# Performance work log

Hardware: AMD Instinct MI355X
Metric: run time of the kernel (lower is better)

Reference implementation:

```python
import jax, jax.numpy as jnp
import numpy as np

DIM, HID, SEQ = 768, 2048, 4096
LR, MOM, WD, THRESH = 1e-3, 0.9, 0.01, 0.1


def _net(p, x):
    W1, b1, W2, b2, W3, b3, W4, b4 = p
    h = jax.nn.relu(x @ W1 + b1)
    h = jax.nn.relu(h @ W2 + b2)
    h = jax.nn.relu(h @ W3 + b3)
    return h @ W4 + b4


def _loss(p, t):
    # t: [dim]; token.unsqueeze(0) then mse_loss (mean over all elements)
    pred = _net(p, t[None, :])
    return jnp.mean((pred - t[None, :]) ** 2)


def _ttt(params, x):
    toks = x[::4]  # `if i % 4 != 0: continue`

    def step(carry, t):
        p, buf, inited = carry
        g = jax.grad(_loss)(p, t)
        surprise = sum(jnp.linalg.norm(gi) for gi in jax.tree_util.tree_leaves(g))
        # momentum buffer: first observation initializes it
        buf_new = jnp.where(inited, MOM * buf + (1.0 - MOM) * surprise, surprise)

        def upd(q):
            qd = jax.tree_util.tree_map(lambda w: w * (1.0 - WD), q)  # weight decay
            g2 = jax.grad(_loss)(qd, t)                                # fresh fwd/bwd
            return jax.tree_util.tree_map(lambda w, gi: w - LR * gi, qd, g2)  # SGD step

        p_new = jax.lax.cond(buf_new > THRESH, upd, lambda q: q, p)
        return (p_new, buf_new, jnp.bool_(True)), None

    (pf, _, _), _ = jax.lax.scan(step, (params, jnp.float32(0.0), jnp.bool_(False)), toks)
    return pf


def setup_inputs() -> dict:
    key = jax.random.key(0)
    ks = jax.random.split(key, 5)

    def lin(k, fi, fo):
        kw, kb = jax.random.split(k)
        w = jax.random.normal(kw, (fi, fo), jnp.float32) / np.sqrt(fi).astype(np.float32)
        b = jax.random.normal(kb, (fo,), jnp.float32) * 0.01
        return w, b

    W1, b1 = lin(ks[0], DIM, HID)
    W2, b2 = lin(ks[1], HID, HID)
    W3, b3 = lin(ks[2], HID, HID)
    W4, b4 = lin(ks[3], HID, DIM)
    x = jax.random.normal(ks[4], (SEQ, DIM), jnp.float32)
    return dict(x=x, W1=W1, b1=b1, W2=W2, b2=b2, W3=W3, b3=b3, W4=W4, b4=b4, do_ttt=1)


def reference(x, W1, b1, W2, b2, W3, b3, W4, b4, do_ttt):
    params = (W1, b1, W2, b2, W3, b3, W4, b4)
    if do_ttt:
        params = _ttt(params, x)
    out = _net(params, x)            # eval pass over full sequence
    return out.mean(axis=0, keepdims=True)  # memory_summary [1, dim]
```

## Files before the change

### kernel.cpp

```cpp
#include <hip/hip_runtime.h>
#include <cstddef>

#define LRC 0.001f
#define DEC 0.99f

static const size_t OFF_Z1P = 0;
static const size_t OFF_Z2P = 65536;
static const size_t OFF_Z2Q = 131072;
static const size_t OFF_Z3P = 196608;
static const size_t OFF_Z3Q = 262144;
static const size_t OFF_Z4P = 327680;
static const size_t OFF_Z4Q = 352256;
static const size_t OFF_H1F = 376832;
static const size_t OFF_H1Q = 378880;
static const size_t OFF_H2F = 380928;
static const size_t OFF_H2Q = 382976;
static const size_t OFF_H3F = 385024;
static const size_t OFF_H3Q = 387072;
static const size_t OFF_D4F = 389120;
static const size_t OFF_D4Q = 389888;
static const size_t OFF_D3F = 390656;
static const size_t OFF_D3Q = 392704;
static const size_t OFF_D2F = 394752;
static const size_t OFF_D2Q = 396800;
static const size_t OFF_D1F = 398848;
static const size_t OFF_D1Q = 400896;
static const size_t OFF_NSQ = 402944;
static const size_t OFF_SL3 = 402960;
static const size_t OFF_SL2 = 403216;
static const size_t OFF_SL1 = 403472;
static const size_t OFF_BUF = 403728;
static const size_t OFF_CONDF = 403730;
static const size_t OFF_MSUM = 403732;
static const size_t OFF_HA  = 428308;
static const size_t OFF_HB  = 2525460;

__device__ inline void fma4(float4& a, float s, const float4& w) {
    a.x += s * w.x; a.y += s * w.y; a.z += s * w.z; a.w += s * w.w;
}

__device__ float block_reduce_512(float v) {
    __shared__ float red[512];
    int t = threadIdx.x;
    red[t] = v;
    __syncthreads();
    for (int s = 256; s > 0; s >>= 1) {
        if (t < s) red[t] += red[t + s];
        __syncthreads();
    }
    float r = red[0];
    __syncthreads();
    return r;
}

__global__ __launch_bounds__(512) void k_fwd1(int step,
                                              const float* __restrict__ xt,
                                              const float* __restrict__ xprev,
                                              float* __restrict__ W1,
                                              float* __restrict__ b1,
                                              float* __restrict__ wsf,
                                              const int* __restrict__ flag) {
    if (*flag == 0) return;
    int b = blockIdx.x;
    int g = b >> 5, p = b & 31;
    int tid = threadIdx.x, w = tid >> 6, lane = tid & 63;
    int c0 = g * 256 + lane * 4;
    int kb = p * 24 + w * 3;

    float4 wv0 = *(const float4*)(W1 + (size_t)(kb + 0) * 2048 + c0);
    float4 wv1 = *(const float4*)(W1 + (size_t)(kb + 1) * 2048 + c0);
    float4 wv2 = *(const float4*)(W1 + (size_t)(kb + 2) * 2048 + c0);
    float a0 = xt[kb + 0], a1 = xt[kb + 1], a2 = xt[kb + 2];
    float4 dv = make_float4(0.f, 0.f, 0.f, 0.f);
    float u0 = 0.f, u1 = 0.f, u2 = 0.f;
    if (step > 0) {
        dv = *(const float4*)(wsf + OFF_D1Q + c0);
        u0 = LRC * xprev[kb + 0]; u1 = LRC * xprev[kb + 1]; u2 = LRC * xprev[kb + 2];
    }

    __shared__ float cnd[4];
    float cond = 0.f;
    if (step > 0) {
        if (w < 3) {
            const float* sl = wsf + (w == 0 ? OFF_SL1 : (w == 1 ? OFF_SL2 : OFF_SL3));
            float v = sl[lane] + sl[lane + 64] + sl[lane + 128] + sl[lane + 192];
#pragma unroll
            for (int off = 32; off > 0; off >>= 1) v += __shfl_down(v, off);
            if (lane == 0) cnd[w] = v;
        }
        __syncthreads();
        float nd1 = sqrtf(cnd[0]), nd2 = sqrtf(cnd[1]), nd3 = sqrtf(cnd[2]);
        float nx = sqrtf(wsf[OFF_NSQ + 0]);
        float nh1 = sqrtf(wsf[OFF_NSQ + 1]);
        float nh2 = sqrtf(wsf[OFF_NSQ + 2]);
        float nh3 = sqrtf(wsf[OFF_NSQ + 3]);
        float nd4 = sqrtf(wsf[OFF_NSQ + 4]);
        float surprise = nx * nd1 + nd1 + nh1 * nd2 + nd2 + nh2 * nd3 + nd3 + nh3 * nd4 + nd4;
        float bufold = wsf[OFF_BUF + ((step - 1) & 1)];
        float bufnew = (step == 1) ? surprise : (0.9f * bufold + 0.1f * surprise);
        cond = (bufnew > 0.1f) ? 1.f : 0.f;
        if (b == 0 && tid == 0) {
            wsf[OFF_BUF + (step & 1)] = bufnew;
            wsf[OFF_CONDF] = cond;
        }
    } else {
        if (b == 0 && tid == 0) wsf[OFF_CONDF] = 0.f;
    }

    if (cond != 0.f) {
        wv0.x = DEC * wv0.x - u0 * dv.x; wv0.y = DEC * wv0.y - u0 * dv.y;
        wv0.z = DEC * wv0.z - u0 * dv.z; wv0.w = DEC * wv0.w - u0 * dv.w;
        wv1.x = DEC * wv1.x - u1 * dv.x; wv1.y = DEC * wv1.y - u1 * dv.y;
        wv1.z = DEC * wv1.z - u1 * dv.z; wv1.w = DEC * wv1.w - u1 * dv.w;
        wv2.x = DEC * wv2.x - u2 * dv.x; wv2.y = DEC * wv2.y - u2 * dv.y;
        wv2.z = DEC * wv2.z - u2 * dv.z; wv2.w = DEC * wv2.w - u2 * dv.w;
        *(float4*)(W1 + (size_t)(kb + 0) * 2048 + c0) = wv0;
        *(float4*)(W1 + (size_t)(kb + 1) * 2048 + c0) = wv1;
        *(float4*)(W1 + (size_t)(kb + 2) * 2048 + c0) = wv2;
        if (b == 0) {
            int c = tid * 4;
            float4 dq = *(const float4*)(wsf + OFF_D1Q + c);
            float4 bv = *(float4*)(b1 + c);
            bv.x = DEC * bv.x - LRC * dq.x; bv.y = DEC * bv.y - LRC * dq.y;
            bv.z = DEC * bv.z - LRC * dq.z; bv.w = DEC * bv.w - LRC * dq.w;
            *(float4*)(b1 + c) = bv;
        }
    }

    float4 acc = make_float4(0.f, 0.f, 0.f, 0.f);
    fma4(acc, a0, wv0); fma4(acc, a1, wv1); fma4(acc, a2, wv2);

    __shared__ float4 red[8][64];
    red[w][lane] = acc;
    __syncthreads();
    if (w == 0) {
        float4 s = red[0][lane];
#pragma unroll
        for (int q = 1; q < 8; ++q) {
            float4 r2 = red[q][lane];
            s.x += r2.x; s.y += r2.y; s.z += r2.z; s.w += r2.w;
        }
        *(float4*)(wsf + OFF_Z1P + (size_t)p * 2048 + c0) = s;
    }
}

__global__ __launch_bounds__(512) void k_fwd2(const float* __restrict__ zinP,
                                              const float* __restrict__ zinQ,
                                              const float* __restrict__ bin,
                                              float* __restrict__ W, int Nout,
                                              float* __restrict__ zoutP,
                                              float* __restrict__ zoutQ,
                                              const float* __restrict__ uprev,
                                              const float* __restrict__ vprev,
                                              float* __restrict__ bl,
                                              const float* __restrict__ wsf,
                                              const int* __restrict__ flag) {
    if (*flag == 0) return;
    int b = blockIdx.x;
    int g = b >> 5, p = b & 31;
    int tid = threadIdx.x, w = tid >> 6, lane = tid & 63;
    bool upd = (wsf[OFF_CONDF] != 0.f);

    __shared__ float hs[64], hq[64], us[64];
    if (tid < 64) {
        int k = p * 64 + tid;
        float s = 0.f;
#pragma unroll 8
        for (int pp = 0; pp < 32; ++pp) s += zinP[pp * 2048 + k];
        float bv = bin[k];
        float h = fmaxf(s + bv, 0.f);
        float hqq;
        if (zinQ) {
            float sq = 0.f;
#pragma unroll 8
            for (int pp = 0; pp < 32; ++pp) sq += zinQ[pp * 2048 + k];
            hqq = fmaxf(DEC * (sq + bv), 0.f);
        } else {
            hqq = DEC * h;
        }
        hs[tid] = h; hq[tid] = hqq;
        us[tid] = upd ? (LRC * uprev[k]) : 0.f;
    }
    __syncthreads();
    int c0 = g * 256 + lane * 4;
    float4 vpv = make_float4(0.f, 0.f, 0.f, 0.f);
    if (upd) vpv = *(const float4*)(vprev + c0);
    float4 ap = make_float4(0.f, 0.f, 0.f, 0.f);
    float4 aq = make_float4(0.f, 0.f, 0.f, 0.f);
    if (upd) {
#pragma unroll
        for (int r = 0; r < 8; ++r) {
            int kk = w * 8 + r;
            float* wp = W + (size_t)(p * 64 + kk) * Nout + c0;
            float4 wv = *(const float4*)wp;
            float u = us[kk];
            wv.x = DEC * wv.x - u * vpv.x; wv.y = DEC * wv.y - u * vpv.y;
            wv.z = DEC * wv.z - u * vpv.z; wv.w = DEC * wv.w - u * vpv.w;
            *(float4*)wp = wv;
            float a = hs[kk], a2 = hq[kk];
            fma4(ap, a, wv);
            fma4(aq, a2, wv);
        }
    } else {
#pragma unroll
        for (int r = 0; r < 8; ++r) {
            int kk = w * 8 + r;
            const float4 wv = *(const float4*)(W + (size_t)(p * 64 + kk) * Nout + c0);
            float a = hs[kk], a2 = hq[kk];
            fma4(ap, a, wv);
            fma4(aq, a2, wv);
        }
    }
    if (upd && b == 0) {
        int c = tid * 4;
        if (c < Nout) {
            float4 dq = *(const float4*)(vprev + c);
            float4 bv = *(float4*)(bl + c);
            bv.x = DEC * bv.x - LRC * dq.x; bv.y = DEC * bv.y - LRC * dq.y;
            bv.z = DEC * bv.z - LRC * dq.z; bv.w = DEC * bv.w - LRC * dq.w;
            *(float4*)(bl + c) = bv;
        }
    }
    __shared__ float4 redP[8][64];
    __shared__ float4 redQ[8][64];
    redP[w][lane] = ap; redQ[w][lane] = aq;
    __syncthreads();
    if (w == 0) {
        float4 sp = redP[0][lane], sq4 = redQ[0][lane];
#pragma unroll
        for (int q = 1; q < 8; ++q) {
            float4 r2 = redP[q][lane]; sp.x += r2.x; sp.y += r2.y; sp.z += r2.z; sp.w += r2.w;
            float4 r3 = redQ[q][lane]; sq4.x += r3.x; sq4.y += r3.y; sq4.z += r3.z; sq4.w += r3.w;
        }
        *(float4*)(zoutP + (size_t)p * Nout + c0) = sp;
        *(float4*)(zoutQ + (size_t)p * Nout + c0) = sq4;
    }
}

__global__ __launch_bounds__(512) void k_fin(float* __restrict__ wsf,
                                             const float* __restrict__ xt,
                                             const float* __restrict__ b1,
                                             const float* __restrict__ b2,
                                             const float* __restrict__ b3,
                                             const float* __restrict__ b4,
                                             const int* __restrict__ flag) {
    if (*flag == 0) return;
    int b = blockIdx.x, tid = threadIdx.x;
    if (b < 16) {
        if (tid < 128) {
            int e = b * 128 + tid;
            float s = 0.f;
#pragma unroll 8
            for (int pp = 0; pp < 32; ++pp) s += wsf[OFF_Z1P + pp * 2048 + e];
            float h = fmaxf(s + b1[e], 0.f);
            wsf[OFF_H1F + e] = h;
            wsf[OFF_H1Q + e] = DEC * h;
        }
    } else if (b < 32) {
        if (tid < 128) {
            int e = (b - 16) * 128 + tid;
            float s = 0.f, sq = 0.f;
#pragma unroll 8
            for (int pp = 0; pp < 32; ++pp) {
                s += wsf[OFF_Z2P + pp * 2048 + e];
                sq += wsf[OFF_Z2Q + pp * 2048 + e];
            }
            float bv = b2[e];
            wsf[OFF_H2F + e] = fmaxf(s + bv, 0.f);
            wsf[OFF_H2Q + e] = fmaxf(DEC * (sq + bv), 0.f);
        }
    } else if (b < 48) {
        if (tid < 128) {
            int e = (b - 32) * 128 + tid;
            float s = 0.f, sq = 0.f;
#pragma unroll 8
            for (int pp = 0; pp < 32; ++pp) {
                s += wsf[OFF_Z3P + pp * 2048 + e];
                sq += wsf[OFF_Z3Q + pp * 2048 + e];
            }
            float bv = b3[e];
            wsf[OFF_H3F + e] = fmaxf(s + bv, 0.f);
            wsf[OFF_H3Q + e] = fmaxf(DEC * (sq + bv), 0.f);
        }
    } else if (b == 48) {
        for (int e = tid; e < 768; e += 512) {
            float s = 0.f, sq = 0.f;
#pragma unroll 8
            for (int pp = 0; pp < 32; ++pp) {
                s += wsf[OFF_Z4P + pp * 768 + e];
                sq += wsf[OFF_Z4Q + pp * 768 + e];
            }
            float bv = b4[e], tv = xt[e];
            float pred = s + bv;
            float predq = DEC * (sq + bv);
            wsf[OFF_D4F + e] = 2.f * (pred - tv) * (1.f / 768.f);
            wsf[OFF_D4Q + e] = 2.f * (predq - tv) * (1.f / 768.f);
        }
    } else if (b == 49) {
        float v = 0.f;
        for (int e = tid; e < 768; e += 512) { float xv = xt[e]; v += xv * xv; }
        float s = block_reduce_512(v);
        if (tid == 0) wsf[OFF_NSQ + 0] = s;
    } else if (b == 50) {
        float v = 0.f;
        for (int e = tid; e < 2048; e += 512) {
            float s = 0.f;
#pragma unroll 8
            for (int pp = 0; pp < 32; ++pp) s += wsf[OFF_Z1P + pp * 2048 + e];
            float h = fmaxf(s + b1[e], 0.f);
            v += h * h;
        }
        float s = block_reduce_512(v);
        if (tid == 0) wsf[OFF_NSQ + 1] = s;
    } else if (b == 51) {
        float v = 0.f;
        for (int e = tid; e < 2048; e += 512) {
            float s = 0.f;
#pragma unroll 8
            for (int pp = 0; pp < 32; ++pp) s += wsf[OFF_Z2P + pp * 2048 + e];
            float h = fmaxf(s + b2[e], 0.f);
            v += h * h;
        }
        float s = block_reduce_512(v);
        if (tid == 0) wsf[OFF_NSQ + 2] = s;
    } else if (b == 52) {
        float v = 0.f;
        for (int e = tid; e < 2048; e += 512) {
            float s = 0.f;
#pragma unroll 8
            for (int pp = 0; pp < 32; ++pp) s += wsf[OFF_Z3P + pp * 2048 + e];
            float h = fmaxf(s + b3[e], 0.f);
            v += h * h;
        }
        float s = block_reduce_512(v);
        if (tid == 0) wsf[OFF_NSQ + 3] = s;
    } else if (b == 53) {
        float v = 0.f;
        for (int e = tid; e < 768; e += 512) {
            float s = 0.f;
#pragma unroll 8
            for (int pp = 0; pp < 32; ++pp) s += wsf[OFF_Z4P + pp * 768 + e];
            float d = 2.f * ((s + b4[e]) - xt[e]) * (1.f / 768.f);
            v += d * d;
        }
        float s = block_reduce_512(v);
        if (tid == 0) wsf[OFF_NSQ + 4] = s;
    }
}

__global__ __launch_bounds__(512) void k_bwd(const float* __restrict__ W, int K,
                                             const float* __restrict__ dinP,
                                             const float* __restrict__ dinQ,
                                             const float* __restrict__ hP,
                                             const float* __restrict__ hQ,
                                             float* __restrict__ doutP,
                                             float* __restrict__ doutQ,
                                             float* __restrict__ slot,
                                             const int* __restrict__ flag) {
    if (*flag == 0) return;
    __shared__ float dsP[2048];
    __shared__ float dsQ[2048];
    int tid = threadIdx.x;
    for (int k = tid; k < K; k += 512) { dsP[k] = dinP[k]; dsQ[k] = dinQ[k]; }
    __syncthreads();
    int w = tid >> 6, lane = tid & 63;
    int j = blockIdx.x * 8 + w;
    const float* row = W + (size_t)j * K;
    float ap = 0.f, aq = 0.f;
    for (int k4 = lane * 4; k4 < K; k4 += 256) {
        const float4 wv = *(const float4*)(row + k4);
        ap += wv.x * dsP[k4] + wv.y * dsP[k4 + 1] + wv.z * dsP[k4 + 2] + wv.w * dsP[k4 + 3];
        aq += wv.x * dsQ[k4] + wv.y * dsQ[k4 + 1] + wv.z * dsQ[k4 + 2] + wv.w * dsQ[k4 + 3];
    }
#pragma unroll
    for (int off = 32; off > 0; off >>= 1) {
        ap += __shfl_down(ap, off);
        aq += __shfl_down(aq, off);
    }
    __shared__ float sqw[8];
    if (lane == 0) {
        float dp = (hP[j] > 0.f) ? ap : 0.f;
        float dq = (hQ[j] > 0.f) ? DEC * aq : 0.f;
        doutP[j] = dp;
        doutQ[j] = dq;
        sqw[w] = dp * dp;
    }
    __syncthreads();
    if (tid == 0) {
        float s = 0.f;
#pragma unroll
        for (int q = 0; q < 8; ++q) s += sqw[q];
        slot[blockIdx.x] = s;
    }
}

__global__ __launch_bounds__(512) void k_upd(int step, float* __restrict__ wsf,
                                             float* __restrict__ W1, float* __restrict__ b1,
                                             float* __restrict__ W2, float* __restrict__ b2,
                                             float* __restrict__ W3, float* __restrict__ b3,
                                             float* __restrict__ W4, float* __restrict__ b4,
                                             const float* __restrict__ xt,
                                             const int* __restrict__ flag) {
    if (*flag == 0) return;
    int tid = threadIdx.x, b = blockIdx.x;
    float s3 = block_reduce_512((tid < 256) ? wsf[OFF_SL3 + tid] : 0.f);
    float s2 = block_reduce_512((tid < 256) ? wsf[OFF_SL2 + tid] : 0.f);
    float s1 = block_reduce_512((tid < 256) ? wsf[OFF_SL1 + tid] : 0.f);
    __shared__ float condsh;
    if (tid == 0) {
        float nx = sqrtf(wsf[OFF_NSQ + 0]);
        float nh1 = sqrtf(wsf[OFF_NSQ + 1]);
        float nh2 = sqrtf(wsf[OFF_NSQ + 2]);
        float nh3 = sqrtf(wsf[OFF_NSQ + 3]);
        float nd4 = sqrtf(wsf[OFF_NSQ + 4]);
        float nd3 = sqrtf(s3), nd2 = sqrtf(s2), nd1 = sqrtf(s1);
        float surprise = nx * nd1 + nd1 + nh1 * nd2 + nd2 + nh2 * nd3 + nd3 + nh3 * nd4 + nd4;
        float bufold = wsf[OFF_BUF + (step & 1)];
        float bufnew = (step == 0) ? surprise : (0.9f * bufold + 0.1f * surprise);
        wsf[OFF_BUF + ((step + 1) & 1)] = bufnew;
        condsh = (bufnew > 0.1f) ? 1.f : 0.f;
    }
    __syncthreads();
    if (condsh == 0.f) return;

    const float* d1q = wsf + OFF_D1Q;
    const float* d2q = wsf + OFF_D2Q;
    const float* d3q = wsf + OFF_D3Q;
    const float* d4q = wsf + OFF_D4Q;
    const float* h1q = wsf + OFF_H1Q;
    const float* h2q = wsf + OFF_H2Q;
    const float* h3q = wsf + OFF_H3Q;
    int c = tid * 4;
    {
        float4 dv = *(const float4*)(d1q + c);
#pragma unroll
        for (int r = 0; r < 3; ++r) {
            int i = b * 3 + r;
            float u = LRC * xt[i];
            float4* wp = (float4*)(W1 + (size_t)i * 2048 + c);
            float4 wv = *wp;
            wv.x = DEC * wv.x - u * dv.x; wv.y = DEC * wv.y - u * dv.y;
            wv.z = DEC * wv.z - u * dv.z; wv.w = DEC * wv.w - u * dv.w;
            *wp = wv;
        }
    }
    {
        float4 dv = *(const float4*)(d2q + c);
#pragma unroll
        for (int r = 0; r < 8; ++r) {
            int i = b * 8 + r;
            float u = LRC * h1q[i];
            float4* wp = (float4*)(W2 + (size_t)i * 2048 + c);
            float4 wv = *wp;
            wv.x = DEC * wv.x - u * dv.x; wv.y = DEC * wv.y - u * dv.y;
            wv.z = DEC * wv.z - u * dv.z; wv.w = DEC * wv.w - u * dv.w;
            *wp = wv;
        }
    }
    {
        float4 dv = *(const float4*)(d3q + c);
#pragma unroll
        for (int r = 0; r < 8; ++r) {
            int i = b * 8 + r;
            float u = LRC * h2q[i];
            float4* wp = (float4*)(W3 + (size_t)i * 2048 + c);
            float4 wv = *wp;
            wv.x = DEC * wv.x - u * dv.x; wv.y = DEC * wv.y - u * dv.y;
            wv.z = DEC * wv.z - u * dv.z; wv.w = DEC * wv.w - u * dv.w;
            *wp = wv;
        }
    }
    if (tid < 192) {
        float4 dv = *(const float4*)(d4q + c);
#pragma unroll
        for (int r = 0; r < 8; ++r) {
            int i = b * 8 + r;
            float u = LRC * h3q[i];
            float4* wp = (float4*)(W4 + (size_t)i * 768 + c);
            float4 wv = *wp;
            wv.x = DEC * wv.x - u * dv.x; wv.y = DEC * wv.y - u * dv.y;
            wv.z = DEC * wv.z - u * dv.z; wv.w = DEC * wv.w - u * dv.w;
            *wp = wv;
        }
    }
    if (b == 0) {
        float4 dv = *(const float4*)(d1q + c);
        float4* bp = (float4*)(b1 + c);
        float4 bv = *bp;
        bv.x = DEC * bv.x - LRC * dv.x; bv.y = DEC * bv.y - LRC * dv.y;
        bv.z = DEC * bv.z - LRC * dv.z; bv.w = DEC * bv.w - LRC * dv.w;
        *bp = bv;
    } else if (b == 1) {
        float4 dv = *(const float4*)(d2q + c);
        float4* bp = (float4*)(b2 + c);
        float4 bv = *bp;
        bv.x = DEC * bv.x - LRC * dv.x; bv.y = DEC * bv.y - LRC * dv.y;
        bv.z = DEC * bv.z - LRC * dv.z; bv.w = DEC * bv.w - LRC * dv.w;
        *bp = bv;
    } else if (b == 2) {
        float4 dv = *(const float4*)(d3q + c);
        float4* bp = (float4*)(b3 + c);
        float4 bv = *bp;
        bv.x = DEC * bv.x - LRC * dv.x; bv.y = DEC * bv.y - LRC * dv.y;
        bv.z = DEC * bv.z - LRC * dv.z; bv.w = DEC * bv.w - LRC * dv.w;
        *bp = bv;
    } else if (b == 3 && tid < 192) {
        float4 dv = *(const float4*)(d4q + c);
        float4* bp = (float4*)(b4 + c);
        float4 bv = *bp;
        bv.x = DEC * bv.x - LRC * dv.x; bv.y = DEC * bv.y - LRC * dv.y;
        bv.z = DEC * bv.z - LRC * dv.z; bv.w = DEC * bv.w - LRC * dv.w;
        *bp = bv;
    }
}

__global__ __launch_bounds__(256) void k_gemm(const float* __restrict__ A,
                                              const float* __restrict__ W,
                                              const float* __restrict__ bias,
                                              float* __restrict__ C,
                                              int M, int N, int K, int do_relu) {
    __shared__ float sA[16][64];
    __shared__ float sB[16][128];
    int bn = blockIdx.x, bm = blockIdx.y;
    int m0 = bm * 64, n0 = bn * 128;
    int tid = threadIdx.x;
    int tx = tid & 31, ty = tid >> 5;
    float acc[8][4];
#pragma unroll
    for (int i = 0; i < 8; ++i)
#pragma unroll
        for (int j = 0; j < 4; ++j) acc[i][j] = 0.f;

    for (int kt = 0; kt < K; kt += 16) {
        {
            int r = tid >> 2, cc = (tid & 3) * 4;
            const float4 a4 = *(const float4*)(A + (size_t)(m0 + r) * K + kt + cc);
            sA[cc + 0][r] = a4.x; sA[cc + 1][r] = a4.y; sA[cc + 2][r] = a4.z; sA[cc + 3][r] = a4.w;
        }
        {
            int r = tid >> 5, cc = (tid & 31) * 4;
            *(float4*)(&sB[r][cc]) = *(const float4*)(W + (size_t)(kt + r) * N + n0 + cc);
            *(float4*)(&sB[r + 8][cc]) = *(const float4*)(W + (size_t)(kt + r + 8) * N + n0 + cc);
        }
        __syncthreads();
#pragma unroll
        for (int k = 0; k < 16; ++k) {
            float av[8];
#pragma unroll
            for (int i = 0; i < 8; ++i) av[i] = sA[k][ty * 8 + i];
            float bx = sB[k][tx * 4 + 0], by = sB[k][tx * 4 + 1];
            float bz = sB[k][tx * 4 + 2], bw = sB[k][tx * 4 + 3];
#pragma unroll
            for (int i = 0; i < 8; ++i) {
                acc[i][0] += av[i] * bx; acc[i][1] += av[i] * by;
                acc[i][2] += av[i] * bz; acc[i][3] += av[i] * bw;
            }
        }
        __syncthreads();
    }
    float bx = bias[n0 + tx * 4 + 0], by = bias[n0 + tx * 4 + 1];
    float bz = bias[n0 + tx * 4 + 2], bw = bias[n0 + tx * 4 + 3];
#pragma unroll
    for (int i = 0; i < 8; ++i) {
        int m = m0 + ty * 8 + i;
        float4 v;
        v.x = acc[i][0] + bx; v.y = acc[i][1] + by;
        v.z = acc[i][2] + bz; v.w = acc[i][3] + bw;
        if (do_relu) {
            v.x = fmaxf(v.x, 0.f); v.y = fmaxf(v.y, 0.f);
            v.z = fmaxf(v.z, 0.f); v.w = fmaxf(v.w, 0.f);
        }
        *(float4*)(C + (size_t)m * N + n0 + tx * 4) = v;
    }
}

__global__ __launch_bounds__(128) void k_colsum(const float* __restrict__ Y,
                                                float* __restrict__ out) {
    int c = blockIdx.x * 128 + threadIdx.x;
    int r0 = blockIdx.y * 128;
    float s = 0.f;
    for (int r = 0; r < 128; ++r) s += Y[(size_t)(r0 + r) * 768 + c];
    out[blockIdx.y * 768 + c] = s;
}

__global__ __launch_bounds__(768) void k_out(const float* __restrict__ msum,
                                             float* __restrict__ out) {
    int c = threadIdx.x;
    float s = 0.f;
#pragma unroll
    for (int i = 0; i < 32; ++i) s += msum[i * 768 + c];
    out[c] = s * (1.f / 4096.f);
}

extern "C" void kernel_launch(void* const* d_in, const int* in_sizes, int n_in,
                              void* d_out, int out_size, void* d_ws, size_t ws_size,
                              hipStream_t stream) {
    const float* x = (const float*)d_in[0];
    float* W1 = (float*)d_in[1];
    float* b1 = (float*)d_in[2];
    float* W2 = (float*)d_in[3];
    float* b2 = (float*)d_in[4];
    float* W3 = (float*)d_in[5];
    float* b3 = (float*)d_in[6];
    float* W4 = (float*)d_in[7];
    float* b4 = (float*)d_in[8];
    const int* flag = (const int*)d_in[9];
    float* wsf = (float*)d_ws;

    for (int s = 0; s < 1024; ++s) {
        const float* xt = x + (size_t)s * 4 * 768;
        const float* xprev = x + (size_t)(s > 0 ? s - 1 : 0) * 4 * 768;
        k_fwd1<<<256, 512, 0, stream>>>(s, xt, xprev, W1, b1, wsf, flag);
        k_fwd2<<<256, 512, 0, stream>>>(wsf + OFF_Z1P, nullptr, b1, W2, 2048,
                                        wsf + OFF_Z2P, wsf + OFF_Z2Q,
                                        wsf + OFF_H1Q, wsf + OFF_D2Q, b2, wsf, flag);
        k_fwd2<<<256, 512, 0, stream>>>(wsf + OFF_Z2P, wsf + OFF_Z2Q, b2, W3, 2048,
                                        wsf + OFF_Z3P, wsf + OFF_Z3Q,
                                        wsf + OFF_H2Q, wsf + OFF_D3Q, b3, wsf, flag);
        k_fwd2<<<96, 512, 0, stream>>>(wsf + OFF_Z3P, wsf + OFF_Z3Q, b3, W4, 768,
                                       wsf + OFF_Z4P, wsf + OFF_Z4Q,
                                       wsf + OFF_H3Q, wsf + OFF_D4Q, b4, wsf, flag);
        k_fin<<<64, 512, 0, stream>>>(wsf, xt, b1, b2, b3, b4, flag);
        k_bwd<<<256, 512, 0, stream>>>(W4, 768, wsf + OFF_D4F, wsf + OFF_D4Q,
                                       wsf + OFF_H3F, wsf + OFF_H3Q,
                                       wsf + OFF_D3F, wsf + OFF_D3Q, wsf + OFF_SL3, flag);
        k_bwd<<<256, 512, 0, stream>>>(W3, 2048, wsf + OFF_D3F, wsf + OFF_D3Q,
                                       wsf + OFF_H2F, wsf + OFF_H2Q,
                                       wsf + OFF_D2F, wsf + OFF_D2Q, wsf + OFF_SL2, flag);
        k_bwd<<<256, 512, 0, stream>>>(W2, 2048, wsf + OFF_D2F, wsf + OFF_D2Q,
                                       wsf + OFF_H1F, wsf + OFF_H1Q,
                                       wsf + OFF_D1F, wsf + OFF_D1Q, wsf + OFF_SL1, flag);
    }
    k_upd<<<256, 512, 0, stream>>>(1023, wsf, W1, b1, W2, b2, W3, b3, W4, b4,
                                   x + (size_t)1023 * 4 * 768, flag);

    float* HA = wsf + OFF_HA;
    float* HB = wsf + OFF_HB;
    for (int ch = 0; ch < 4; ++ch) {
        const float* Xc = x + (size_t)ch * 1024 * 768;
        k_gemm<<<dim3(16, 16), 256, 0, stream>>>(Xc, W1, b1, HA, 1024, 2048, 768, 1);
        k_gemm<<<dim3(16, 16), 256, 0, stream>>>(HA, W2, b2, HB, 1024, 2048, 2048, 1);
        k_gemm<<<dim3(16, 16), 256, 0, stream>>>(HB, W3, b3, HA, 1024, 2048, 2048, 1);
        k_gemm<<<dim3(6, 16), 256, 0, stream>>>(HA, W4, b4, HB, 1024, 768, 2048, 0);
        k_colsum<<<dim3(6, 8), 128, 0, stream>>>(HB, wsf + OFF_MSUM + (size_t)ch * 8 * 768);
    }
    k_out<<<1, 768, 0, stream>>>(wsf + OFF_MSUM, (float*)d_out);
}
```

Baseline: 64.93 ms.

## Fuse per-step TTT kernels into one persistent kernel with grid barriers

Replaces the roughly 8 kernel launches per scan step (over 8000 in total) with a single persistent 256-block kernel that moves between phases through a hierarchical atomic grid barrier. The finalize phase is spread across idle blocks during the layer-4 forward, and the layer-4 backward is fused with the computation of its output gradient. The goal is to remove per-launch overhead and the gaps between launches. In exchange it depends on all 256 blocks being resident at once, and each step now pays the cost of spinning on global atomic barriers.

Measured after the change: 211.7 ms. 226% more time.

```diff
diff --git a/kernel.cpp b/kernel.cpp
--- a/kernel.cpp
+++ b/kernel.cpp
@@ -3,6 +3,7 @@
 
 #define LRC 0.001f
 #define DEC 0.99f
+#define NBLK 256
 
 static const size_t OFF_Z1P = 0;
 static const size_t OFF_Z2P = 65536;
@@ -35,17 +36,16 @@
 static const size_t OFF_HA  = 428308;
 static const size_t OFF_HB  = 2525460;
 
-__device__ inline void fma4(float4& a, float s, const float4& w) {
+__device__ __forceinline__ void fma4(float4& a, float s, const float4& w) {
     a.x += s * w.x; a.y += s * w.y; a.z += s * w.z; a.w += s * w.w;
 }
 
-__device__ float block_reduce_512(float v) {
-    __shared__ float red[512];
+__device__ __forceinline__ float block_reduce_512s(float v, float* red) {
     int t = threadIdx.x;
     red[t] = v;
     __syncthreads();
-    for (int s = 256; s > 0; s >>= 1) {
-        if (t < s) red[t] += red[t + s];
+    for (int st = 256; st > 0; st >>= 1) {
+        if (t < st) red[t] += red[t + st];
         __syncthreads();
     }
     float r = red[0];
@@ -53,14 +53,35 @@
     return r;
 }
 
-__global__ __launch_bounds__(512) void k_fwd1(int step,
-                                              const float* __restrict__ xt,
-                                              const float* __restrict__ xprev,
-                                              float* __restrict__ W1,
-                                              float* __restrict__ b1,
-                                              float* __restrict__ wsf,
-                                              const int* __restrict__ flag) {
-    if (*flag == 0) return;
+__device__ __forceinline__ void gbar(unsigned* bar) {
+    __syncthreads();
+    if (threadIdx.x == 0) {
+        __threadfence();
+        unsigned g = __hip_atomic_load(bar, __ATOMIC_RELAXED, __HIP_MEMORY_SCOPE_AGENT);
+        unsigned* grp = bar + 64 + ((blockIdx.x >> 4) << 5);
+        if (__hip_atomic_fetch_add(grp, 1u, __ATOMIC_ACQ_REL, __HIP_MEMORY_SCOPE_AGENT) == 15u) {
+            if (__hip_atomic_fetch_add(bar + 32, 1u, __ATOMIC_ACQ_REL, __HIP_MEMORY_SCOPE_AGENT) == 15u) {
+#pragma unroll
+                for (int i = 0; i < 16; ++i)
+                    __hip_atomic_store(bar + 64 + (i << 5), 0u, __ATOMIC_RELAXED, __HIP_MEMORY_SCOPE_AGENT);
+                __hip_atomic_store(bar + 32, 0u, __ATOMIC_RELAXED, __HIP_MEMORY_SCOPE_AGENT);
+                __hip_atomic_store(bar, g + 1u, __ATOMIC_RELEASE, __HIP_MEMORY_SCOPE_AGENT);
+            }
+        }
+        while (__hip_atomic_load(bar, __ATOMIC_RELAXED, __HIP_MEMORY_SCOPE_AGENT) == g)
+            __builtin_amdgcn_s_sleep(2);
+        __threadfence();
+    }
+    __syncthreads();
+}
+
+__device__ __forceinline__ void ph_fwd1(int step,
+                                        const float* __restrict__ xt,
+                                        const float* __restrict__ xprev,
+                                        float* __restrict__ W1,
+                                        float* __restrict__ b1,
+                                        float* __restrict__ wsf,
+                                        float* smem) {
     int b = blockIdx.x;
     int g = b >> 5, p = b & 31;
     int tid = threadIdx.x, w = tid >> 6, lane = tid & 63;
@@ -78,7 +99,7 @@
         u0 = LRC * xprev[kb + 0]; u1 = LRC * xprev[kb + 1]; u2 = LRC * xprev[kb + 2];
     }
 
-    __shared__ float cnd[4];
+    float* cnd = smem + 2048;
     float cond = 0.f;
     if (step > 0) {
         if (w < 3) {
@@ -130,38 +151,37 @@
     float4 acc = make_float4(0.f, 0.f, 0.f, 0.f);
     fma4(acc, a0, wv0); fma4(acc, a1, wv1); fma4(acc, a2, wv2);
 
-    __shared__ float4 red[8][64];
-    red[w][lane] = acc;
+    float4* red4 = (float4*)smem;
+    red4[w * 64 + lane] = acc;
     __syncthreads();
     if (w == 0) {
-        float4 s = red[0][lane];
+        float4 s = red4[lane];
 #pragma unroll
         for (int q = 1; q < 8; ++q) {
-            float4 r2 = red[q][lane];
+            float4 r2 = red4[q * 64 + lane];
             s.x += r2.x; s.y += r2.y; s.z += r2.z; s.w += r2.w;
         }
         *(float4*)(wsf + OFF_Z1P + (size_t)p * 2048 + c0) = s;
     }
 }
 
-__global__ __launch_bounds__(512) void k_fwd2(const float* __restrict__ zinP,
-                                              const float* __restrict__ zinQ,
-                                              const float* __restrict__ bin,
-                                              float* __restrict__ W, int Nout,
-                                              float* __restrict__ zoutP,
-                                              float* __restrict__ zoutQ,
-                                              const float* __restrict__ uprev,
-                                              const float* __restrict__ vprev,
-                                              float* __restrict__ bl,
-                                              const float* __restrict__ wsf,
-                                              const int* __restrict__ flag) {
-    if (*flag == 0) return;
-    int b = blockIdx.x;
+__device__ __forceinline__ void ph_fwd2(int b,
+                                        const float* __restrict__ zinP,
+                                        const float* __restrict__ zinQ,
+                                        const float* __restrict__ bin,
+                                        float* __restrict__ W, int Nout,
+                                        float* __restrict__ zoutP,
+                                        float* __restrict__ zoutQ,
+                                        const float* __restrict__ uprev,
+                                        const float* __restrict__ vprev,
+                                        float* __restrict__ bl,
+                                        const float* __restrict__ wsf,
+                                        float* smem) {
     int g = b >> 5, p = b & 31;
     int tid = threadIdx.x, w = tid >> 6, lane = tid & 63;
     bool upd = (wsf[OFF_CONDF] != 0.f);
 
-    __shared__ float hs[64], hq[64], us[64];
+    float* hs = smem; float* hq = smem + 64; float* us = smem + 128;
     if (tid < 64) {
         int k = p * 64 + tid;
         float s = 0.f;
@@ -221,150 +241,173 @@
             *(float4*)(bl + c) = bv;
         }
     }
-    __shared__ float4 redP[8][64];
-    __shared__ float4 redQ[8][64];
-    redP[w][lane] = ap; redQ[w][lane] = aq;
+    float4* redP = (float4*)(smem + 256);
+    float4* redQ = (float4*)(smem + 2304);
+    redP[w * 64 + lane] = ap; redQ[w * 64 + lane] = aq;
     __syncthreads();
     if (w == 0) {
-        float4 sp = redP[0][lane], sq4 = redQ[0][lane];
+        float4 sp = redP[lane], sq4 = redQ[lane];
 #pragma unroll
         for (int q = 1; q < 8; ++q) {
-            float4 r2 = redP[q][lane]; sp.x += r2.x; sp.y += r2.y; sp.z += r2.z; sp.w += r2.w;
-            float4 r3 = redQ[q][lane]; sq4.x += r3.x; sq4.y += r3.y; sq4.z += r3.z; sq4.w += r3.w;
+            float4 r2 = redP[q * 64 + lane]; sp.x += r2.x; sp.y += r2.y; sp.z += r2.z; sp.w += r2.w;
+            float4 r3 = redQ[q * 64 + lane]; sq4.x += r3.x; sq4.y += r3.y; sq4.z += r3.z; sq4.w += r3.w;
         }
         *(float4*)(zoutP + (size_t)p * Nout + c0) = sp;
         *(float4*)(zoutQ + (size_t)p * Nout + c0) = sq4;
     }
 }
 
-__global__ __launch_bounds__(512) void k_fin(float* __restrict__ wsf,
-                                             const float* __restrict__ xt,
-                                             const float* __restrict__ b1,
-                                             const float* __restrict__ b2,
-                                             const float* __restrict__ b3,
-                                             const float* __restrict__ b4,
-                                             const int* __restrict__ flag) {
-    if (*flag == 0) return;
-    int b = blockIdx.x, tid = threadIdx.x;
-    if (b < 16) {
-        if (tid < 128) {
-            int e = b * 128 + tid;
-            float s = 0.f;
+__device__ __forceinline__ void ph_finH1(int bb, const float* __restrict__ b1v,
+                                         float* __restrict__ wsf) {
+    int tid = threadIdx.x;
+    if (tid < 128) {
+        int e = bb * 128 + tid;
+        float s = 0.f;
 #pragma unroll 8
-            for (int pp = 0; pp < 32; ++pp) s += wsf[OFF_Z1P + pp * 2048 + e];
-            float h = fmaxf(s + b1[e], 0.f);
-            wsf[OFF_H1F + e] = h;
-            wsf[OFF_H1Q + e] = DEC * h;
-        }
-    } else if (b < 32) {
-        if (tid < 128) {
-            int e = (b - 16) * 128 + tid;
-            float s = 0.f, sq = 0.f;
+        for (int pp = 0; pp < 32; ++pp) s += wsf[OFF_Z1P + pp * 2048 + e];
+        float h = fmaxf(s + b1v[e], 0.f);
+        wsf[OFF_H1F + e] = h;
+        wsf[OFF_H1Q + e] = DEC * h;
+    }
+}
+
+__device__ __forceinline__ void ph_finH2(int bb, const float* __restrict__ b2v,
+                                         float* __restrict__ wsf) {
+    int tid = threadIdx.x;
+    if (tid < 128) {
+        int e = bb * 128 + tid;
+        float s = 0.f, sq = 0.f;
 #pragma unroll 8
-            for (int pp = 0; pp < 32; ++pp) {
-                s += wsf[OFF_Z2P + pp * 2048 + e];
-                sq += wsf[OFF_Z2Q + pp * 2048 + e];
-            }
-            float bv = b2[e];
-            wsf[OFF_H2F + e] = fmaxf(s + bv, 0.f);
-            wsf[OFF_H2Q + e] = fmaxf(DEC * (sq + bv), 0.f);
-        }
-    } else if (b < 48) {
-        if (tid < 128) {
-            int e = (b - 32) * 128 + tid;
-            float s = 0.f, sq = 0.f;
+        for (int pp = 0; pp < 32; ++pp) {
+            s += wsf[OFF_Z2P + pp * 2048 + e];
+            sq += wsf[OFF_Z2Q + pp * 2048 + e];
+        }
+        float bv = b2v[e];
+        wsf[OFF_H2F + e] = fmaxf(s + bv, 0.f);
+        wsf[OFF_H2Q + e] = fmaxf(DEC * (sq + bv), 0.f);
+    }
+}
+
+__device__ __forceinline__ void ph_normX(const float* __restrict__ xt,
+                                         float* __restrict__ wsf, float* smem) {
+    int tid = threadIdx.x;
+    float v = 0.f;
+    for (int e = tid; e < 768; e += 512) { float xv = xt[e]; v += xv * xv; }
+    float s = block_reduce_512s(v, smem);
+    if (tid == 0) wsf[OFF_NSQ + 0] = s;
+}
+
+__device__ __forceinline__ void ph_normH(const float* __restrict__ zin,
+                                         const float* __restrict__ bias, int idx,
+                                         float* __restrict__ wsf, float* smem) {
+    int tid = threadIdx.x;
+    float v = 0.f;
+    for (int e = tid; e < 2048; e += 512) {
+        float s = 0.f;
 #pragma unroll 8
-            for (int pp = 0; pp < 32; ++pp) {
-                s += wsf[OFF_Z3P + pp * 2048 + e];
-                sq += wsf[OFF_Z3Q + pp * 2048 + e];
-            }
-            float bv = b3[e];
-            wsf[OFF_H3F + e] = fmaxf(s + bv, 0.f);
-            wsf[OFF_H3Q + e] = fmaxf(DEC * (sq + bv), 0.f);
-        }
-    } else if (b == 48) {
+        for (int pp = 0; pp < 32; ++pp) s += zin[pp * 2048 + e];
+        float h = fmaxf(s + bias[e], 0.f);
+        v += h * h;
+    }
+    float s2 = block_reduce_512s(v, smem);
+    if (tid == 0) wsf[OFF_NSQ + idx] = s2;
+}
+
+__device__ __forceinline__ void ph_bwd4(const float* __restrict__ W4,
+                                        const float* __restrict__ b3v,
+                                        const float* __restrict__ b4v,
+                                        const float* __restrict__ xt,
+                                        float* __restrict__ wsf, float* smem) {
+    float* dsP = smem;
+    float* dsQ = smem + 2048;
+    float* red = smem + 4096;
+    float* sqw = smem + 4608;
+    float* h3f = smem + 4616;
+    float* h3q = smem + 4624;
+    int tid = threadIdx.x, b = blockIdx.x;
+
+    if (tid < 8) {
+        int j = b * 8 + tid;
+        float s = 0.f, sq = 0.f;
+#pragma unroll 8
+        for (int pp = 0; pp < 32; ++pp) {
+            s += wsf[OFF_Z3P + pp * 2048 + j];
+            sq += wsf[OFF_Z3Q + pp * 2048 + j];
+        }
+        float bv = b3v[j];
+        float hf = fmaxf(s + bv, 0.f);
+        float hqv = fmaxf(DEC * (sq + bv), 0.f);
+        wsf[OFF_H3F + j] = hf; wsf[OFF_H3Q + j] = hqv;
+        h3f[tid] = hf; h3q[tid] = hqv;
+    }
+    for (int e = tid; e < 768; e += 512) {
+        float s = 0.f, sq = 0.f;
+#pragma unroll 8
+        for (int pp = 0; pp < 32; ++pp) {
+            s += wsf[OFF_Z4P + pp * 768 + e];
+            sq += wsf[OFF_Z4Q + pp * 768 + e];
+        }
+        float bv = b4v[e], tv = xt[e];
+        dsP[e] = 2.f * ((s + bv) - tv) * (1.f / 768.f);
+        dsQ[e] = 2.f * (DEC * (sq + bv) - tv) * (1.f / 768.f);
+    }
+    __syncthreads();
+    if (b == 0) {
         for (int e = tid; e < 768; e += 512) {
-            float s = 0.f, sq = 0.f;
-#pragma unroll 8
-            for (int pp = 0; pp < 32; ++pp) {
-                s += wsf[OFF_Z4P + pp * 768 + e];
-                sq += wsf[OFF_Z4Q + pp * 768 + e];
-            }
-            float bv = b4[e], tv = xt[e];
-            float pred = s + bv;
-            float predq = DEC * (sq + bv);
-            wsf[OFF_D4F + e] = 2.f * (pred - tv) * (1.f / 768.f);
-            wsf[OFF_D4Q + e] = 2.f * (predq - tv) * (1.f / 768.f);
-        }
-    } else if (b == 49) {
+            wsf[OFF_D4F + e] = dsP[e];
+            wsf[OFF_D4Q + e] = dsQ[e];
+        }
         float v = 0.f;
-        for (int e = tid; e < 768; e += 512) { float xv = xt[e]; v += xv * xv; }
-        float s = block_reduce_512(v);
-        if (tid == 0) wsf[OFF_NSQ + 0] = s;
-    } else if (b == 50) {
-        float v = 0.f;
-        for (int e = tid; e < 2048; e += 512) {
-            float s = 0.f;
-#pragma unroll 8
-            for (int pp = 0; pp < 32; ++pp) s += wsf[OFF_Z1P + pp * 2048 + e];
-            float h = fmaxf(s + b1[e], 0.f);
-            v += h * h;
-        }
-        float s = block_reduce_512(v);
-        if (tid == 0) wsf[OFF_NSQ + 1] = s;
-    } else if (b == 51) {
-        float v = 0.f;
-        for (int e = tid; e < 2048; e += 512) {
-            float s = 0.f;
-#pragma unroll 8
-            for (int pp = 0; pp < 32; ++pp) s += wsf[OFF_Z2P + pp * 2048 + e];
-            float h = fmaxf(s + b2[e], 0.f);
-            v += h * h;
-        }
-        float s = block_reduce_512(v);
-        if (tid == 0) wsf[OFF_NSQ + 2] = s;
-    } else if (b == 52) {
-        float v = 0.f;
-        for (int e = tid; e < 2048; e += 512) {
-            float s = 0.f;
-#pragma unroll 8
-            for (int pp = 0; pp < 32; ++pp) s += wsf[OFF_Z3P + pp * 2048 + e];
-            float h = fmaxf(s + b3[e], 0.f);
-            v += h * h;
-        }
-        float s = block_reduce_512(v);
-        if (tid == 0) wsf[OFF_NSQ + 3] = s;
-    } else if (b == 53) {
-        float v = 0.f;
-        for (int e = tid; e < 768; e += 512) {
-            float s = 0.f;
-#pragma unroll 8
-            for (int pp = 0; pp < 32; ++pp) s += wsf[OFF_Z4P + pp * 768 + e];
-            float d = 2.f * ((s + b4[e]) - xt[e]) * (1.f / 768.f);
-            v += d * d;
-        }
-        float s = block_reduce_512(v);
+        for (int e = tid; e < 768; e += 512) { float d = dsP[e]; v += d * d; }
+        float s = block_reduce_512s(v, red);
         if (tid == 0) wsf[OFF_NSQ + 4] = s;
     }
-}
-
-__global__ __launch_bounds__(512) void k_bwd(const float* __restrict__ W, int K,
-                                             const float* __restrict__ dinP,
-                                             const float* __restrict__ dinQ,
-                                             const float* __restrict__ hP,
-                                             const float* __restrict__ hQ,
-                                             float* __restrict__ doutP,
-                                             float* __restrict__ doutQ,
-                                             float* __restrict__ slot,
-                                             const int* __restrict__ flag) {
-    if (*flag == 0) return;
-    __shared__ float dsP[2048];
-    __shared__ float dsQ[2048];
+    int w = tid >> 6, lane = tid & 63;
+    const float* row = W4 + (size_t)(b * 8 + w) * 768;
+    float apv = 0.f, aqv = 0.f;
+    for (int k4 = lane * 4; k4 < 768; k4 += 256) {
+        const float4 wv = *(const float4*)(row + k4);
+        apv += wv.x * dsP[k4] + wv.y * dsP[k4 + 1] + wv.z * dsP[k4 + 2] + wv.w * dsP[k4 + 3];
+        aqv += wv.x * dsQ[k4] + wv.y * dsQ[k4 + 1] + wv.z * dsQ[k4 + 2] + wv.w * dsQ[k4 + 3];
+    }
+#pragma unroll
+    for (int off = 32; off > 0; off >>= 1) {
+        apv += __shfl_down(apv, off);
+        aqv += __shfl_down(aqv, off);
+    }
+    if (lane == 0) {
+        float dp = (h3f[w] > 0.f) ? apv : 0.f;
+        float dq = (h3q[w] > 0.f) ? DEC * aqv : 0.f;
+        wsf[OFF_D3F + b * 8 + w] = dp;
+        wsf[OFF_D3Q + b * 8 + w] = dq;
+        sqw[w] = dp * dp;
+    }
+    __syncthreads();
+    if (tid == 0) {
+        float s = 0.f;
+#pragma unroll
+        for (int q = 0; q < 8; ++q) s += sqw[q];
+        wsf[OFF_SL3 + b] = s;
+    }
+}
+
+__device__ __forceinline__ void ph_bwd(int b, const float* __restrict__ W, int K,
+                                       const float* __restrict__ dinP,
+                                       const float* __restrict__ dinQ,
+                                       const float* __restrict__ hP,
+                                       const float* __restrict__ hQ,
+                                       float* __restrict__ doutP,
+                                       float* __restrict__ doutQ,
+                                       float* __restrict__ slot,
+                                       float* smem) {
+    float* dsP = smem;
+    float* dsQ = smem + 2048;
+    float* sqw = smem + 4096;
     int tid = threadIdx.x;
     for (int k = tid; k < K; k += 512) { dsP[k] = dinP[k]; dsQ[k] = dinQ[k]; }
     __syncthreads();
     int w = tid >> 6, lane = tid & 63;
-    int j = blockIdx.x * 8 + w;
+    int j = b * 8 + w;
     const float* row = W + (size_t)j * K;
     float ap = 0.f, aq = 0.f;
     for (int k4 = lane * 4; k4 < K; k4 += 256) {
@@ -377,7 +420,6 @@
         ap += __shfl_down(ap, off);
         aq += __shfl_down(aq, off);
     }
-    __shared__ float sqw[8];
     if (lane == 0) {
         float dp = (hP[j] > 0.f) ? ap : 0.f;
         float dq = (hQ[j] > 0.f) ? DEC * aq : 0.f;
@@ -390,23 +432,22 @@
         float s = 0.f;
 #pragma unroll
         for (int q = 0; q < 8; ++q) s += sqw[q];
-        slot[blockIdx.x] = s;
-    }
-}
-
-__global__ __launch_bounds__(512) void k_upd(int step, float* __restrict__ wsf,
-                                             float* __restrict__ W1, float* __restrict__ b1,
-                                             float* __restrict__ W2, float* __restrict__ b2,
-                                             float* __restrict__ W3, float* __restrict__ b3,
-                                             float* __restrict__ W4, float* __restrict__ b4,
-                                             const float* __restrict__ xt,
-                                             const int* __restrict__ flag) {
-    if (*flag == 0) return;
+        slot[b] = s;
+    }
+}
+
+__device__ __forceinline__ void ph_upd(int step, float* __restrict__ wsf,
+                                       float* __restrict__ W1, float* __restrict__ b1,
+                                       float* __restrict__ W2, float* __restrict__ b2,
+                                       float* __restrict__ W3, float* __restrict__ b3,
+                                       float* __restrict__ W4, float* __restrict__ b4,
+                                       const float* __restrict__ xt, float* smem) {
     int tid = threadIdx.x, b = blockIdx.x;
-    float s3 = block_reduce_512((tid < 256) ? wsf[OFF_SL3 + tid] : 0.f);
-    float s2 = block_reduce_512((tid < 256) ? wsf[OFF_SL2 + tid] : 0.f);
-    float s1 = block_reduce_512((tid < 256) ? wsf[OFF_SL1 + tid] : 0.f);
-    __shared__ float condsh;
+    float* red = smem;
+    float s3 = block_reduce_512s((tid < 256) ? wsf[OFF_SL3 + tid] : 0.f, red);
+    float s2 = block_reduce_512s((tid < 256) ? wsf[OFF_SL2 + tid] : 0.f, red);
+    float s1 = block_reduce_512s((tid < 256) ? wsf[OFF_SL1 + tid] : 0.f, red);
+    float* condp = smem + 512;
     if (tid == 0) {
         float nx = sqrtf(wsf[OFF_NSQ + 0]);
         float nh1 = sqrtf(wsf[OFF_NSQ + 1]);
@@ -418,10 +459,10 @@
         float bufold = wsf[OFF_BUF + (step & 1)];
         float bufnew = (step == 0) ? surprise : (0.9f * bufold + 0.1f * surprise);
         wsf[OFF_BUF + ((step + 1) & 1)] = bufnew;
-        condsh = (bufnew > 0.1f) ? 1.f : 0.f;
-    }
-    __syncthreads();
-    if (condsh == 0.f) return;
+        condp[0] = (bufnew > 0.1f) ? 1.f : 0.f;
+    }
+    __syncthreads();
+    if (condp[0] == 0.f) return;
 
     const float* d1q = wsf + OFF_D1Q;
     const float* d2q = wsf + OFF_D2Q;
@@ -514,6 +555,61 @@
     }
 }
 
+__global__ __launch_bounds__(1024) void k_zero(unsigned* __restrict__ bar) {
+    bar[threadIdx.x] = 0u;
+}
+
+__global__ __launch_bounds__(512) void k_scan(const float* __restrict__ x,
+                                              float* __restrict__ W1, float* __restrict__ b1,
+                                              float* __restrict__ W2, float* __restrict__ b2,
+                                              float* __restrict__ W3, float* __restrict__ b3,
+                                              float* __restrict__ W4, float* __restrict__ b4,
+                                              float* __restrict__ wsf,
+                                              const int* __restrict__ flag) {
+    if (*flag == 0) return;
+    __shared__ float smem[4640];
+    unsigned* bar = (unsigned*)(wsf + OFF_HA);
+    int b = blockIdx.x;
+    for (int s = 0; s < 1024; ++s) {
+        const float* xt = x + (size_t)s * 3072;
+        const float* xprev = x + (size_t)(s > 0 ? s - 1 : 0) * 3072;
+        ph_fwd1(s, xt, xprev, W1, b1, wsf, smem);
+        gbar(bar);
+        ph_fwd2(b, wsf + OFF_Z1P, nullptr, b1, W2, 2048, wsf + OFF_Z2P, wsf + OFF_Z2Q,
+                wsf + OFF_H1Q, wsf + OFF_D2Q, b2, wsf, smem);
+        gbar(bar);
+        ph_fwd2(b, wsf + OFF_Z2P, wsf + OFF_Z2Q, b2, W3, 2048, wsf + OFF_Z3P, wsf + OFF_Z3Q,
+                wsf + OFF_H2Q, wsf + OFF_D3Q, b3, wsf, smem);
+        gbar(bar);
+        if (b < 96) {
+            ph_fwd2(b, wsf + OFF_Z3P, wsf + OFF_Z3Q, b3, W4, 768, wsf + OFF_Z4P, wsf + OFF_Z4Q,
+                    wsf + OFF_H3Q, wsf + OFF_D4Q, b4, wsf, smem);
+        } else if (b < 112) {
+            ph_finH1(b - 96, b1, wsf);
+        } else if (b < 128) {
+            ph_finH2(b - 112, b2, wsf);
+        } else if (b == 144) {
+            ph_normX(xt, wsf, smem);
+        } else if (b == 145) {
+            ph_normH(wsf + OFF_Z1P, b1, 1, wsf, smem);
+        } else if (b == 146) {
+            ph_normH(wsf + OFF_Z2P, b2, 2, wsf, smem);
+        } else if (b == 147) {
+            ph_normH(wsf + OFF_Z3P, b3, 3, wsf, smem);
+        }
+        gbar(bar);
+        ph_bwd4(W4, b3, b4, xt, wsf, smem);
+        gbar(bar);
+        ph_bwd(b, W3, 2048, wsf + OFF_D3F, wsf + OFF_D3Q, wsf + OFF_H2F, wsf + OFF_H2Q,
+               wsf + OFF_D2F, wsf + OFF_D2Q, wsf + OFF_SL2, smem);
+        gbar(bar);
+        ph_bwd(b, W2, 2048, wsf + OFF_D2F, wsf + OFF_D2Q, wsf + OFF_H1F, wsf + OFF_H1Q,
+               wsf + OFF_D1F, wsf + OFF_D1Q, wsf + OFF_SL1, smem);
+        gbar(bar);
+    }
+    ph_upd(1023, wsf, W1, b1, W2, b2, W3, b3, W4, b4, x + (size_t)1023 * 3072, smem);
+}
+
 __global__ __launch_bounds__(256) void k_gemm(const float* __restrict__ A,
                                               const float* __restrict__ W,
                                               const float* __restrict__ bias,
@@ -607,32 +703,10 @@
     const int* flag = (const int*)d_in[9];
     float* wsf = (float*)d_ws;
 
-    for (int s = 0; s < 1024; ++s) {
-        const float* xt = x + (size_t)s * 4 * 768;
-        const float* xprev = x + (size_t)(s > 0 ? s - 1 : 0) * 4 * 768;
-        k_fwd1<<<256, 512, 0, stream>>>(s, xt, xprev, W1, b1, wsf, flag);
-        k_fwd2<<<256, 512, 0, stream>>>(wsf + OFF_Z1P, nullptr, b1, W2, 2048,
-                                        wsf + OFF_Z2P, wsf + OFF_Z2Q,
-                                        wsf + OFF_H1Q, wsf + OFF_D2Q, b2, wsf, flag);
-        k_fwd2<<<256, 512, 0, stream>>>(wsf + OFF_Z2P, wsf + OFF_Z2Q, b2, W3, 2048,
-                                        wsf + OFF_Z3P, wsf + OFF_Z3Q,
-                                        wsf + OFF_H2Q, wsf + OFF_D3Q, b3, wsf, flag);
-        k_fwd2<<<96, 512, 0, stream>>>(wsf + OFF_Z3P, wsf + OFF_Z3Q, b3, W4, 768,
-                                       wsf + OFF_Z4P, wsf + OFF_Z4Q,
-                                       wsf + OFF_H3Q, wsf + OFF_D4Q, b4, wsf, flag);
-        k_fin<<<64, 512, 0, stream>>>(wsf, xt, b1, b2, b3, b4, flag);
-        k_bwd<<<256, 512, 0, stream>>>(W4, 768, wsf + OFF_D4F, wsf + OFF_D4Q,
-                                       wsf + OFF_H3F, wsf + OFF_H3Q,
-                                       wsf + OFF_D3F, wsf + OFF_D3Q, wsf + OFF_SL3, flag);
-        k_bwd<<<256, 512, 0, stream>>>(W3, 2048, wsf + OFF_D3F, wsf + OFF_D3Q,
-                                       wsf + OFF_H2F, wsf + OFF_H2Q,
-                                       wsf + OFF_D2F, wsf + OFF_D2Q, wsf + OFF_SL2, flag);
-        k_bwd<<<256, 512, 0, stream>>>(W2, 2048, wsf + OFF_D2F, wsf + OFF_D2Q,
-                                       wsf + OFF_H1F, wsf + OFF_H1Q,
-                                       wsf + OFF_D1F, wsf + OFF_D1Q, wsf + OFF_SL1, flag);
-    }
-    k_upd<<<256, 512, 0, stream>>>(1023, wsf, W1, b1, W2, b2, W3, b3, W4, b4,
-                                   x + (size_t)1023 * 4 * 768, flag);
+    unsigned* bar = (unsigned*)(wsf + OFF_HA);
+    k_zero<<<1, 1024, 0, stream>>>(bar);
+
+    k_scan<<<256, 512, 0, stream>>>(x, W1, b1, W2, b2, W3, b3, W4, b4, wsf, flag);
 
     float* HA = wsf + OFF_HA;
     float* HB = wsf + OFF_HB;
```
